# Performance work log

Hardware: AMD Instinct MI355X
Metric: run time of the kernel (lower is better)

## Reference

```python
import jax, jax.numpy as jnp
import numpy as np

NS_ITERS = 15
EPS = 1e-6


def _sqrtm(x):
    """Newton-Schulz matrix square root, 15 fixed iterations (Lin & Maji)."""
    dim = x.shape[0]
    norm = jnp.linalg.norm(x)  # Frobenius norm
    Y = x / norm
    I = jnp.eye(dim, dtype=x.dtype)
    Z = I
    for _ in range(NS_ITERS):
        T = 0.5 * (3.0 * I - Z @ Y)
        Y = Y @ T
        Z = T @ Z
    return Y * jnp.sqrt(norm)


def _gram(X):
    a, b = X.shape
    return (X @ X.T + EPS * jnp.eye(a, dtype=X.dtype)) / b


def setup_inputs() -> dict:
    key = jax.random.key(0)
    k1, k2 = jax.random.split(key)
    inp = jax.random.normal(k1, (1, 512, 256, 256), dtype=jnp.float32)
    tgt = jax.random.normal(k2, (1, 512, 256, 256), dtype=jnp.float32)
    return {"input": inp, "target_feature": tgt}


def reference(input, target_feature):
    a, b, c, d = input.shape
    n = a * b
    # --- target statistics (precomputed in __init__ of the torch module) ---
    Xt = target_feature.reshape(n, c * d)
    Mt = Xt.mean(axis=1)                     # [n]
    Gt = _gram(Xt - Mt[:, None])             # [n, n]
    sqrt_Gt = _sqrtm(Gt)                     # [n, n]
    # --- current statistics ---
    X = input.reshape(n, c * d)
    M = X.mean(axis=1)
    G = _gram(X - M[:, None])
    sqrt_G = _sqrtm(G)
    # mse(reduction='sum') on means + Bures/Wasserstein SPD distance
    loss = jnp.sum((M - Mt) ** 2)
    loss = loss + jnp.trace(G + Gt) - 2.0 * jnp.trace(sqrt_G @ sqrt_Gt)
    return loss / b
```

## Files before the change

### kernel.cpp

```cpp
#include <hip/hip_runtime.h>
#include <math.h>

#define KDIM 65536
#define MATF 262144
#define NK 16
#define CHUNK 4096
#define EPSG 1e-6

using bf16x8 = __attribute__((ext_vector_type(8))) __bf16;
using f32x4  = __attribute__((ext_vector_type(4))) float;


__global__ __launch_bounds__(256) void k_means(const float* __restrict__ X,
                                               const float* __restrict__ Xt,
                                               float* __restrict__ M) {
  const int row = blockIdx.x, inp = blockIdx.y;
  const float4* p = (const float4*)((inp ? Xt : X) + (size_t)row * KDIM);
  double s = 0.0;
  for (int i = threadIdx.x; i < KDIM / 4; i += 256) {
    float4 v = p[i];
    s += (double)v.x + (double)v.y + (double)v.z + (double)v.w;
  }
  __shared__ double sm[256];
  sm[threadIdx.x] = s;
  __syncthreads();
  for (int o = 128; o > 0; o >>= 1) {
    if (threadIdx.x < o) sm[threadIdx.x] += sm[threadIdx.x + o];
    __syncthreads();
  }
  if (threadIdx.x == 0) M[inp * 512 + row] = (float)(sm[0] * (1.0 / KDIM));
}

__device__ __forceinline__ void cvt8(float4 a, float4 b, bf16x8& hi, bf16x8& lo) {
  float f[8] = {a.x, a.y, a.z, a.w, b.x, b.y, b.z, b.w};
#pragma unroll
  for (int e = 0; e < 8; ++e) {
    __bf16 h = (__bf16)f[e];
    hi[e] = h;
    lo[e] = (__bf16)(f[e] - (float)h);
  }
}

__global__ __launch_bounds__(256, 2) void k_gram(const float* __restrict__ X,
                                                 const float* __restrict__ Xt,
                                                 float* __restrict__ Gp) {
  int rem = blockIdx.x, ti = 0;
  while (rem >= 4 - ti) { rem -= 4 - ti; ++ti; }
  const int tj = ti + rem;
  const int chunk = blockIdx.y, inp = blockIdx.z;
  const float* __restrict__ A = inp ? Xt : X;
  float* __restrict__ C = Gp + ((size_t)(inp * NK + chunk)) * MATF;
  const bool diag = (ti == tj);

  __shared__ bf16x8 AhV[512], AlV[512], BhV[512], BlV[512];

  const int t = threadIdx.x;
  const int srow = t & 127, skh = t >> 7;
  const int sbase = ((srow >> 4) << 6) + (skh << 5) + (srow & 15);

  const float* pa = A + (size_t)(ti * 128 + srow) * KDIM + (size_t)chunk * CHUNK + skh * 16;
  const float* pb = A + (size_t)(tj * 128 + srow) * KDIM + (size_t)chunk * CHUNK + skh * 16;

  const int wave = t >> 6, lane = t & 63;
  const int wy = (wave >> 1) * 64, wx = (wave & 1) * 64;

  f32x4 acc[4][4];
#pragma unroll
  for (int i = 0; i < 4; ++i)
#pragma unroll
    for (int j = 0; j < 4; ++j) acc[i][j] = (f32x4){0.f, 0.f, 0.f, 0.f};

  for (int ks = 0; ks < CHUNK; ks += 32) {
    {
      float4 v0 = *(const float4*)(pa + ks);
      float4 v1 = *(const float4*)(pa + ks + 4);
      float4 v2 = *(const float4*)(pa + ks + 8);
      float4 v3 = *(const float4*)(pa + ks + 12);
      bf16x8 h, l;
      cvt8(v0, v1, h, l); AhV[sbase] = h; AlV[sbase] = l;
      cvt8(v2, v3, h, l); AhV[sbase + 16] = h; AlV[sbase + 16] = l;
      if (!diag) {
        v0 = *(const float4*)(pb + ks);
        v1 = *(const float4*)(pb + ks + 4);
        v2 = *(const float4*)(pb + ks + 8);
        v3 = *(const float4*)(pb + ks + 12);
        cvt8(v0, v1, h, l); BhV[sbase] = h; BlV[sbase] = l;
        cvt8(v2, v3, h, l); BhV[sbase + 16] = h; BlV[sbase + 16] = l;
      }
    }
    __syncthreads();
    const bf16x8* __restrict__ Bh = diag ? AhV : BhV;
    const bf16x8* __restrict__ Bl = diag ? AlV : BlV;
    bf16x8 ah[4], al[4], bh[4], bl[4];
#pragma unroll
    for (int g = 0; g < 4; ++g) {
      ah[g] = AhV[((wave >> 1) * 4 + g) * 64 + lane];
      al[g] = AlV[((wave >> 1) * 4 + g) * 64 + lane];
      bh[g] = Bh[((wave & 1) * 4 + g) * 64 + lane];
      bl[g] = Bl[((wave & 1) * 4 + g) * 64 + lane];
    }
#pragma unroll
    for (int i = 0; i < 4; ++i)
#pragma unroll
      for (int j = 0; j < 4; ++j) {
        acc[i][j] = __builtin_amdgcn_mfma_f32_16x16x32_bf16(ah[i], bh[j], acc[i][j], 0, 0, 0);
        acc[i][j] = __builtin_amdgcn_mfma_f32_16x16x32_bf16(al[i], bh[j], acc[i][j], 0, 0, 0);
        acc[i][j] = __builtin_amdgcn_mfma_f32_16x16x32_bf16(ah[i], bl[j], acc[i][j], 0, 0, 0);
      }
    __syncthreads();
  }
  const int r4 = (lane >> 4) * 4, fc = lane & 15;
#pragma unroll
  for (int i = 0; i < 4; ++i) {
    const int grow = ti * 128 + wy + i * 16 + r4;
#pragma unroll
    for (int j = 0; j < 4; ++j) {
      const int gcol = tj * 128 + wx + j * 16 + fc;
#pragma unroll
      for (int r = 0; r < 4; ++r)
        C[(size_t)(grow + r) * 512 + gcol] = acc[i][j][r];
    }
  }
}

__global__ __launch_bounds__(256) void k_gfin(const float* __restrict__ Gp,
                                              const float* __restrict__ M,
                                              float* __restrict__ G,
                                              double* __restrict__ S) {
  const int inp = blockIdx.y;
  const int idx = blockIdx.x * 256 + threadIdx.x;
  const int i = idx >> 9, j = idx & 511;
  double n2 = 0.0, tr = 0.0;
  float* g = G + (size_t)inp * MATF;
  if (i <= j) {
    double sum = 0.0;
    const float* p = Gp + (size_t)inp * NK * MATF + idx;
#pragma unroll
    for (int c = 0; c < NK; ++c) sum += (double)p[(size_t)c * MATF];
    sum -= 65536.0 * (double)M[inp * 512 + i] * (double)M[inp * 512 + j];
    if (i == j) sum += EPSG;
    float v = (float)(sum * (1.0 / 65536.0));
    g[idx] = v;
    if (i < j) { g[(size_t)j * 512 + i] = v; n2 = 2.0 * (double)v * (double)v; }
    else       { n2 = (double)v * (double)v; tr = (double)v; }
  }
  __shared__ double s1[256], s2[256];
  s1[threadIdx.x] = n2; s2[threadIdx.x] = tr;
  __syncthreads();
  for (int o = 128; o > 0; o >>= 1) {
    if (threadIdx.x < o) { s1[threadIdx.x] += s1[threadIdx.x + o]; s2[threadIdx.x] += s2[threadIdx.x + o]; }
    __syncthreads();
  }
  if (threadIdx.x == 0) { atomicAdd(&S[inp], s1[0]); atomicAdd(&S[2 + inp], s2[0]); }
}

__global__ __launch_bounds__(256) void k_nsinit(const float* __restrict__ G,
                                                float* __restrict__ Y,
                                                float* __restrict__ Z,
                                                const double* __restrict__ S) {
  const int inp = blockIdx.y;
  const int idx = blockIdx.x * 256 + threadIdx.x;
  const float norm = (float)sqrt(S[inp]);
  Y[(size_t)(inp * 2 + 0) * MATF + idx] = G[(size_t)inp * MATF + idx] / norm;
  Y[(size_t)(inp * 2 + 1) * MATF + idx] = 0.0f;
  Z[(size_t)(inp * 2 + 0) * MATF + idx] = ((idx >> 9) == (idx & 511)) ? 1.0f : 0.0f;
  Z[(size_t)(inp * 2 + 1) * MATF + idx] = 0.0f;
}

__device__ __forceinline__ void gemm_ns(const float* __restrict__ A0, const float* __restrict__ A1,
                                        const float* __restrict__ B0, const float* __restrict__ B1,
                                        const float* __restrict__ E0, const float* __restrict__ E1,
                                        float* __restrict__ C, int k0, int mode) {
  __shared__ __align__(16) float As[64][68];
  __shared__ __align__(16) float Bs[64][68];
  const int t = threadIdx.x;
  const int tx = t & 15, ty = t >> 4;
  const int bi = blockIdx.x, bj = blockIdx.y;
  const int ar = t & 63, akq = t >> 6;
  const int bkr = t >> 2, bcs = (t & 3) * 16;

  const float* pa0 = A0 + (size_t)(bi * 64 + ar) * 512 + k0 + akq * 16;
  const float* pa1 = A1 + (size_t)(bi * 64 + ar) * 512 + k0 + akq * 16;
  const float* pb0 = B0 + (size_t)(k0 + bkr) * 512 + bj * 64 + bcs;
  const float* pb1 = B1 + (size_t)(k0 + bkr) * 512 + bj * 64 + bcs;

  float acc[4][4] = {};
  for (int ks = 0; ks < 256; ks += 64) {
#pragma unroll
    for (int q = 0; q < 4; ++q) {
      float4 va = *(const float4*)(pa0 + ks + q * 4);
      float4 vb = *(const float4*)(pa1 + ks + q * 4);
      const int kk = akq * 16 + q * 4;
      As[kk + 0][ar] = va.x + vb.x; As[kk + 1][ar] = va.y + vb.y;
      As[kk + 2][ar] = va.z + vb.z; As[kk + 3][ar] = va.w + vb.w;
    }
#pragma unroll
    for (int q = 0; q < 4; ++q) {
      float4 va = *(const float4*)(pb0 + (size_t)ks * 512 + q * 4);
      float4 vb = *(const float4*)(pb1 + (size_t)ks * 512 + q * 4);
      va.x += vb.x; va.y += vb.y; va.z += vb.z; va.w += vb.w;
      *(float4*)&Bs[bkr][bcs + q * 4] = va;
    }
    __syncthreads();
#pragma unroll 16
    for (int kk = 0; kk < 64; ++kk) {
      const float4 av = *(const float4*)&As[kk][ty << 2];
      const float4 bv = *(const float4*)&Bs[kk][tx << 2];
      acc[0][0] += av.x * bv.x; acc[0][1] += av.x * bv.y; acc[0][2] += av.x * bv.z; acc[0][3] += av.x * bv.w;
      acc[1][0] += av.y * bv.x; acc[1][1] += av.y * bv.y; acc[1][2] += av.y * bv.z; acc[1][3] += av.y * bv.w;
      acc[2][0] += av.z * bv.x; acc[2][1] += av.z * bv.y; acc[2][2] += av.z * bv.z; acc[2][3] += av.z * bv.w;
      acc[3][0] += av.w * bv.x; acc[3][1] += av.w * bv.y; acc[3][2] += av.w * bv.z; acc[3][3] += av.w * bv.w;
    }
    __syncthreads();
  }
#pragma unroll
  for (int r = 0; r < 4; ++r) {
    const int row = bi * 64 + (ty << 2) + r;
    const size_t off = (size_t)row * 512 + bj * 64 + (tx << 2);
    float4 v = make_float4(acc[r][0], acc[r][1], acc[r][2], acc[r][3]);
    if (mode != 0) {
      v.x *= -0.5f; v.y *= -0.5f; v.z *= -0.5f; v.w *= -0.5f;
      if (mode == 1) {
        float4 e0 = *(const float4*)(E0 + off);
        float4 e1 = *(const float4*)(E1 + off);
        v.x += 1.5f * (e0.x + e1.x); v.y += 1.5f * (e0.y + e1.y);
        v.z += 1.5f * (e0.z + e1.z); v.w += 1.5f * (e0.w + e1.w);
      }
    }
    *(float4*)&C[off] = v;
  }
}

__global__ __launch_bounds__(256) void k_ns_W(const float* __restrict__ Y,
                                              const float* __restrict__ Z,
                                              float* __restrict__ W) {
  const int mat = blockIdx.z >> 1, part = blockIdx.z & 1;
  const float* Zp = Z + (size_t)mat * 2 * MATF;
  const float* Yp = Y + (size_t)mat * 2 * MATF;
  gemm_ns(Zp, Zp + MATF, Yp, Yp + MATF, Yp, Yp,
          W + (size_t)(mat * 2 + part) * MATF, part * 256, 0);
}

__global__ __launch_bounds__(256) void k_ns_YZ(const float* __restrict__ Y,
                                               const float* __restrict__ Z,
                                               const float* __restrict__ W,
                                               float* __restrict__ Yn,
                                               float* __restrict__ Zn) {
  const int mat = blockIdx.z >> 2, which = (blockIdx.z >> 1) & 1, part = blockIdx.z & 1;
  const float* Yp = Y + (size_t)mat * 2 * MATF;
  const float* Zp = Z + (size_t)mat * 2 * MATF;
  const float* Wp = W + (size_t)mat * 2 * MATF;
  const int mode = (part == 0) ? 1 : 2;
  const float *a0, *a1, *b0, *b1, *e0, *e1;
  float* c;
  if (which == 0) {
    a0 = Yp; a1 = Yp + MATF; b0 = Wp; b1 = Wp + MATF; e0 = Yp; e1 = Yp + MATF;
    c = Yn + (size_t)(mat * 2 + part) * MATF;
  } else {
    a0 = Wp; a1 = Wp + MATF; b0 = Zp; b1 = Zp + MATF; e0 = Zp; e1 = Zp + MATF;
    c = Zn + (size_t)(mat * 2 + part) * MATF;
  }
  gemm_ns(a0, a1, b0, b1, e0, e1, c, part * 256, mode);
}

__global__ __launch_bounds__(256) void k_cross(const float* __restrict__ Y,
                                               double* __restrict__ S) {
  const float* YA0 = Y;            const float* YA1 = Y + MATF;
  const float* YB0 = Y + 2 * MATF; const float* YB1 = Y + 3 * MATF;
  const int base = (blockIdx.x * 256 + threadIdx.x) * 4;
  double s = 0.0;
#pragma unroll
  for (int r = 0; r < 4; ++r) {
    const int id = base + r;
    const int i = id >> 9, j = id & 511;
    const int jd = j * 512 + i;
    s += ((double)YA0[id] + (double)YA1[id]) * ((double)YB0[jd] + (double)YB1[jd]);
  }
  __shared__ double sm[256];
  sm[threadIdx.x] = s;
  __syncthreads();
  for (int o = 128; o > 0; o >>= 1) {
    if (threadIdx.x < o) sm[threadIdx.x] += sm[threadIdx.x + o];
    __syncthreads();
  }
  if (threadIdx.x == 0) atomicAdd(&S[4], sm[0]);
}

__global__ __launch_bounds__(256) void k_final(const float* __restrict__ M,
                                               const double* __restrict__ S,
                                               float* __restrict__ out) {
  double s = 0.0;
  for (int i = threadIdx.x; i < 512; i += 256) {
    double d = (double)M[i] - (double)M[512 + i];
    s += d * d;
  }
  __shared__ double sm[256];
  sm[threadIdx.x] = s;
  __syncthreads();
  for (int o = 128; o > 0; o >>= 1) {
    if (threadIdx.x < o) sm[threadIdx.x] += sm[threadIdx.x + o];
    __syncthreads();
  }
  if (threadIdx.x == 0) {
    double scale = sqrt(sqrt(S[0]) * sqrt(S[1]));
    double loss = sm[0] + S[2] + S[3] - 2.0 * scale * S[4];
    out[0] = (float)(loss / 512.0);
  }
}

extern "C" void kernel_launch(void* const* d_in, const int* in_sizes, int n_in,
                              void* d_out, int out_size, void* d_ws, size_t ws_size,
                              hipStream_t stream) {
  const float* X = (const float*)d_in[0];
  const float* Xt = (const float*)d_in[1];
  char* wsb = (char*)d_ws;
  float* Mv = (float*)wsb;
  double* S = (double*)(wsb + 4096);
  float* G = (float*)(wsb + 8192);
  float* big = (float*)(wsb + 8192 + 2 * (size_t)MATF * 4);
  float* Gp = big;
  float* Yb[2] = { big, big + 4 * (size_t)MATF };
  float* Zb[2] = { big + 8 * (size_t)MATF, big + 12 * (size_t)MATF };
  float* W = big + 16 * (size_t)MATF;

  hipMemsetAsync(S, 0, 16 * sizeof(double), stream);
  k_means<<<dim3(512, 2), 256, 0, stream>>>(X, Xt, Mv);
  k_gram<<<dim3(10, NK, 2), 256, 0, stream>>>(X, Xt, Gp);
  k_gfin<<<dim3(1024, 2), 256, 0, stream>>>(Gp, Mv, G, S);
  k_nsinit<<<dim3(1024, 2), 256, 0, stream>>>(G, Yb[0], Zb[0], S);
  int cur = 0;
  for (int it = 0; it < 15; ++it) {
    k_ns_W<<<dim3(8, 8, 4), 256, 0, stream>>>(Yb[cur], Zb[cur], W);
    k_ns_YZ<<<dim3(8, 8, 8), 256, 0, stream>>>(Yb[cur], Zb[cur], W, Yb[1 - cur], Zb[1 - cur]);
    cur ^= 1;
  }
  k_cross<<<dim3(256), 256, 0, stream>>>(Yb[cur], S);
  k_final<<<dim3(1), 256, 0, stream>>>(Mv, S, (float*)d_out);
}
```

Before: 1.416 ms.

## Fuse means into gram, prefetch loads, and run Newton-Schulz in one cooperative kernel

The separate row-mean kernel is removed: row sums are accumulated in the diagonal gram tiles and added to a global buffer with atomics. Global loads in the gram kernel are register-prefetched one step ahead. The K split doubles when the workspace is large enough. The 30 Newton-Schulz launches, together with init, cross-trace and final reduction, are replaced by one cooperative persistent kernel that uses grid.sync between phases, and the Y/Z K-split partial buffers are dropped in favour of full-K GEMMs. This removes a full read pass over the inputs and the launch overhead, at the cost of grid-wide barriers and fewer, longer-running blocks per GEMM.

```diff
diff --git a/kernel.cpp b/kernel.cpp
--- a/kernel.cpp
+++ b/kernel.cpp
@@ -1,35 +1,16 @@
 #include <hip/hip_runtime.h>
+#include <hip/hip_cooperative_groups.h>
 #include <math.h>
+
+namespace cg = cooperative_groups;
 
 #define KDIM 65536
 #define MATF 262144
-#define NK 16
-#define CHUNK 4096
 #define EPSG 1e-6
 
 using bf16x8 = __attribute__((ext_vector_type(8))) __bf16;
 using f32x4  = __attribute__((ext_vector_type(4))) float;
 
-
-__global__ __launch_bounds__(256) void k_means(const float* __restrict__ X,
-                                               const float* __restrict__ Xt,
-                                               float* __restrict__ M) {
-  const int row = blockIdx.x, inp = blockIdx.y;
-  const float4* p = (const float4*)((inp ? Xt : X) + (size_t)row * KDIM);
-  double s = 0.0;
-  for (int i = threadIdx.x; i < KDIM / 4; i += 256) {
-    float4 v = p[i];
-    s += (double)v.x + (double)v.y + (double)v.z + (double)v.w;
-  }
-  __shared__ double sm[256];
-  sm[threadIdx.x] = s;
-  __syncthreads();
-  for (int o = 128; o > 0; o >>= 1) {
-    if (threadIdx.x < o) sm[threadIdx.x] += sm[threadIdx.x + o];
-    __syncthreads();
-  }
-  if (threadIdx.x == 0) M[inp * 512 + row] = (float)(sm[0] * (1.0 / KDIM));
-}
 
 __device__ __forceinline__ void cvt8(float4 a, float4 b, bf16x8& hi, bf16x8& lo) {
   float f[8] = {a.x, a.y, a.z, a.w, b.x, b.y, b.z, b.w};
@@ -43,13 +24,15 @@
 
 __global__ __launch_bounds__(256, 2) void k_gram(const float* __restrict__ X,
                                                  const float* __restrict__ Xt,
-                                                 float* __restrict__ Gp) {
+                                                 float* __restrict__ Gp,
+                                                 double* __restrict__ Msum,
+                                                 int nk, int chunk) {
   int rem = blockIdx.x, ti = 0;
   while (rem >= 4 - ti) { rem -= 4 - ti; ++ti; }
   const int tj = ti + rem;
-  const int chunk = blockIdx.y, inp = blockIdx.z;
+  const int chunkIdx = blockIdx.y, inp = blockIdx.z;
   const float* __restrict__ A = inp ? Xt : X;
-  float* __restrict__ C = Gp + ((size_t)(inp * NK + chunk)) * MATF;
+  float* __restrict__ C = Gp + ((size_t)(inp * nk + chunkIdx)) * MATF;
   const bool diag = (ti == tj);
 
   __shared__ bf16x8 AhV[512], AlV[512], BhV[512], BlV[512];
@@ -58,8 +41,8 @@
   const int srow = t & 127, skh = t >> 7;
   const int sbase = ((srow >> 4) << 6) + (skh << 5) + (srow & 15);
 
-  const float* pa = A + (size_t)(ti * 128 + srow) * KDIM + (size_t)chunk * CHUNK + skh * 16;
-  const float* pb = A + (size_t)(tj * 128 + srow) * KDIM + (size_t)chunk * CHUNK + skh * 16;
+  const float* pa = A + (size_t)(ti * 128 + srow) * KDIM + (size_t)chunkIdx * chunk + skh * 16;
+  const float* pb = A + (size_t)(tj * 128 + srow) * KDIM + (size_t)chunkIdx * chunk + skh * 16;
 
   const int wave = t >> 6, lane = t & 63;
   const int wy = (wave >> 1) * 64, wx = (wave & 1) * 64;
@@ -70,25 +53,45 @@
 #pragma unroll
     for (int j = 0; j < 4; ++j) acc[i][j] = (f32x4){0.f, 0.f, 0.f, 0.f};
 
-  for (int ks = 0; ks < CHUNK; ks += 32) {
+  float4 ra0 = *(const float4*)(pa);
+  float4 ra1 = *(const float4*)(pa + 4);
+  float4 ra2 = *(const float4*)(pa + 8);
+  float4 ra3 = *(const float4*)(pa + 12);
+  float4 rb0, rb1, rb2, rb3;
+  if (!diag) {
+    rb0 = *(const float4*)(pb);
+    rb1 = *(const float4*)(pb + 4);
+    rb2 = *(const float4*)(pb + 8);
+    rb3 = *(const float4*)(pb + 12);
+  }
+  float rsum = 0.f;
+
+  for (int ks = 0; ks < chunk; ks += 32) {
     {
-      float4 v0 = *(const float4*)(pa + ks);
-      float4 v1 = *(const float4*)(pa + ks + 4);
-      float4 v2 = *(const float4*)(pa + ks + 8);
-      float4 v3 = *(const float4*)(pa + ks + 12);
       bf16x8 h, l;
-      cvt8(v0, v1, h, l); AhV[sbase] = h; AlV[sbase] = l;
-      cvt8(v2, v3, h, l); AhV[sbase + 16] = h; AlV[sbase + 16] = l;
+      cvt8(ra0, ra1, h, l); AhV[sbase] = h; AlV[sbase] = l;
+      cvt8(ra2, ra3, h, l); AhV[sbase + 16] = h; AlV[sbase + 16] = l;
+      if (diag) {
+        rsum += ra0.x + ra0.y + ra0.z + ra0.w + ra1.x + ra1.y + ra1.z + ra1.w +
+                ra2.x + ra2.y + ra2.z + ra2.w + ra3.x + ra3.y + ra3.z + ra3.w;
+      } else {
+        cvt8(rb0, rb1, h, l); BhV[sbase] = h; BlV[sbase] = l;
+        cvt8(rb2, rb3, h, l); BhV[sbase + 16] = h; BlV[sbase + 16] = l;
+      }
+    }
+    __syncthreads();
+    if (ks + 32 < chunk) {
+      ra0 = *(const float4*)(pa + ks + 32);
+      ra1 = *(const float4*)(pa + ks + 36);
+      ra2 = *(const float4*)(pa + ks + 40);
+      ra3 = *(const float4*)(pa + ks + 44);
       if (!diag) {
-        v0 = *(const float4*)(pb + ks);
-        v1 = *(const float4*)(pb + ks + 4);
-        v2 = *(const float4*)(pb + ks + 8);
-        v3 = *(const float4*)(pb + ks + 12);
-        cvt8(v0, v1, h, l); BhV[sbase] = h; BlV[sbase] = l;
-        cvt8(v2, v3, h, l); BhV[sbase + 16] = h; BlV[sbase + 16] = l;
-      }
-    }
-    __syncthreads();
+        rb0 = *(const float4*)(pb + ks + 32);
+        rb1 = *(const float4*)(pb + ks + 36);
+        rb2 = *(const float4*)(pb + ks + 40);
+        rb3 = *(const float4*)(pb + ks + 44);
+      }
+    }
     const bf16x8* __restrict__ Bh = diag ? AhV : BhV;
     const bf16x8* __restrict__ Bl = diag ? AlV : BlV;
     bf16x8 ah[4], al[4], bh[4], bl[4];
@@ -109,6 +112,7 @@
       }
     __syncthreads();
   }
+  if (diag) atomicAdd(&Msum[inp * 512 + ti * 128 + srow], (double)rsum);
   const int r4 = (lane >> 4) * 4, fc = lane & 15;
 #pragma unroll
   for (int i = 0; i < 4; ++i) {
@@ -124,9 +128,9 @@
 }
 
 __global__ __launch_bounds__(256) void k_gfin(const float* __restrict__ Gp,
-                                              const float* __restrict__ M,
+                                              const double* __restrict__ Msum,
                                               float* __restrict__ G,
-                                              double* __restrict__ S) {
+                                              double* __restrict__ S, int nk) {
   const int inp = blockIdx.y;
   const int idx = blockIdx.x * 256 + threadIdx.x;
   const int i = idx >> 9, j = idx & 511;
@@ -134,10 +138,9 @@
   float* g = G + (size_t)inp * MATF;
   if (i <= j) {
     double sum = 0.0;
-    const float* p = Gp + (size_t)inp * NK * MATF + idx;
-#pragma unroll
-    for (int c = 0; c < NK; ++c) sum += (double)p[(size_t)c * MATF];
-    sum -= 65536.0 * (double)M[inp * 512 + i] * (double)M[inp * 512 + j];
+    const float* p = Gp + (size_t)inp * nk * MATF + idx;
+    for (int c = 0; c < nk; ++c) sum += (double)p[(size_t)c * MATF];
+    sum -= Msum[inp * 512 + i] * Msum[inp * 512 + j] * (1.0 / 65536.0);
     if (i == j) sum += EPSG;
     float v = (float)(sum * (1.0 / 65536.0));
     g[idx] = v;
@@ -154,51 +157,41 @@
   if (threadIdx.x == 0) { atomicAdd(&S[inp], s1[0]); atomicAdd(&S[2 + inp], s2[0]); }
 }
 
-__global__ __launch_bounds__(256) void k_nsinit(const float* __restrict__ G,
-                                                float* __restrict__ Y,
-                                                float* __restrict__ Z,
-                                                const double* __restrict__ S) {
-  const int inp = blockIdx.y;
-  const int idx = blockIdx.x * 256 + threadIdx.x;
-  const float norm = (float)sqrt(S[inp]);
-  Y[(size_t)(inp * 2 + 0) * MATF + idx] = G[(size_t)inp * MATF + idx] / norm;
-  Y[(size_t)(inp * 2 + 1) * MATF + idx] = 0.0f;
-  Z[(size_t)(inp * 2 + 0) * MATF + idx] = ((idx >> 9) == (idx & 511)) ? 1.0f : 0.0f;
-  Z[(size_t)(inp * 2 + 1) * MATF + idx] = 0.0f;
-}
-
-__device__ __forceinline__ void gemm_ns(const float* __restrict__ A0, const float* __restrict__ A1,
-                                        const float* __restrict__ B0, const float* __restrict__ B1,
-                                        const float* __restrict__ E0, const float* __restrict__ E1,
-                                        float* __restrict__ C, int k0, int mode) {
-  __shared__ __align__(16) float As[64][68];
-  __shared__ __align__(16) float Bs[64][68];
+__device__ __forceinline__ void gemm64(const float* __restrict__ A0, const float* __restrict__ A1,
+                                       const float* __restrict__ B0, const float* __restrict__ B1,
+                                       const float* __restrict__ E, float* __restrict__ C,
+                                       float (*As)[68], float (*Bs)[68],
+                                       int ti, int tj, int k0, int klen, int mode) {
   const int t = threadIdx.x;
   const int tx = t & 15, ty = t >> 4;
-  const int bi = blockIdx.x, bj = blockIdx.y;
   const int ar = t & 63, akq = t >> 6;
-  const int bkr = t >> 2, bcs = (t & 3) * 16;
-
-  const float* pa0 = A0 + (size_t)(bi * 64 + ar) * 512 + k0 + akq * 16;
-  const float* pa1 = A1 + (size_t)(bi * 64 + ar) * 512 + k0 + akq * 16;
-  const float* pb0 = B0 + (size_t)(k0 + bkr) * 512 + bj * 64 + bcs;
-  const float* pb1 = B1 + (size_t)(k0 + bkr) * 512 + bj * 64 + bcs;
+  const int bkr = t >> 2, bcs = (t & 3) << 4;
+
+  const float* pa0 = A0 + (size_t)(ti * 64 + ar) * 512 + k0 + akq * 16;
+  const float* pa1 = A1 ? A1 + (size_t)(ti * 64 + ar) * 512 + k0 + akq * 16 : nullptr;
+  const float* pb0 = B0 + (size_t)(k0 + bkr) * 512 + tj * 64 + bcs;
+  const float* pb1 = B1 ? B1 + (size_t)(k0 + bkr) * 512 + tj * 64 + bcs : nullptr;
 
   float acc[4][4] = {};
-  for (int ks = 0; ks < 256; ks += 64) {
+  for (int ks = 0; ks < klen; ks += 64) {
 #pragma unroll
     for (int q = 0; q < 4; ++q) {
       float4 va = *(const float4*)(pa0 + ks + q * 4);
-      float4 vb = *(const float4*)(pa1 + ks + q * 4);
+      if (pa1) {
+        float4 vb = *(const float4*)(pa1 + ks + q * 4);
+        va.x += vb.x; va.y += vb.y; va.z += vb.z; va.w += vb.w;
+      }
       const int kk = akq * 16 + q * 4;
-      As[kk + 0][ar] = va.x + vb.x; As[kk + 1][ar] = va.y + vb.y;
-      As[kk + 2][ar] = va.z + vb.z; As[kk + 3][ar] = va.w + vb.w;
+      As[kk + 0][ar] = va.x; As[kk + 1][ar] = va.y;
+      As[kk + 2][ar] = va.z; As[kk + 3][ar] = va.w;
     }
 #pragma unroll
     for (int q = 0; q < 4; ++q) {
       float4 va = *(const float4*)(pb0 + (size_t)ks * 512 + q * 4);
-      float4 vb = *(const float4*)(pb1 + (size_t)ks * 512 + q * 4);
-      va.x += vb.x; va.y += vb.y; va.z += vb.z; va.w += vb.w;
+      if (pb1) {
+        float4 vb = *(const float4*)(pb1 + (size_t)ks * 512 + q * 4);
+        va.x += vb.x; va.y += vb.y; va.z += vb.z; va.w += vb.w;
+      }
       *(float4*)&Bs[bkr][bcs + q * 4] = va;
     }
     __syncthreads();
@@ -215,96 +208,101 @@
   }
 #pragma unroll
   for (int r = 0; r < 4; ++r) {
-    const int row = bi * 64 + (ty << 2) + r;
-    const size_t off = (size_t)row * 512 + bj * 64 + (tx << 2);
+    const int row = ti * 64 + (ty << 2) + r;
+    const size_t off = (size_t)row * 512 + tj * 64 + (tx << 2);
     float4 v = make_float4(acc[r][0], acc[r][1], acc[r][2], acc[r][3]);
-    if (mode != 0) {
-      v.x *= -0.5f; v.y *= -0.5f; v.z *= -0.5f; v.w *= -0.5f;
-      if (mode == 1) {
-        float4 e0 = *(const float4*)(E0 + off);
-        float4 e1 = *(const float4*)(E1 + off);
-        v.x += 1.5f * (e0.x + e1.x); v.y += 1.5f * (e0.y + e1.y);
-        v.z += 1.5f * (e0.z + e1.z); v.w += 1.5f * (e0.w + e1.w);
-      }
+    if (mode == 1) {
+      float4 e = *(const float4*)(E + off);
+      v.x = 1.5f * e.x - 0.5f * v.x; v.y = 1.5f * e.y - 0.5f * v.y;
+      v.z = 1.5f * e.z - 0.5f * v.z; v.w = 1.5f * e.w - 0.5f * v.w;
     }
     *(float4*)&C[off] = v;
   }
 }
 
-__global__ __launch_bounds__(256) void k_ns_W(const float* __restrict__ Y,
-                                              const float* __restrict__ Z,
-                                              float* __restrict__ W) {
-  const int mat = blockIdx.z >> 1, part = blockIdx.z & 1;
-  const float* Zp = Z + (size_t)mat * 2 * MATF;
-  const float* Yp = Y + (size_t)mat * 2 * MATF;
-  gemm_ns(Zp, Zp + MATF, Yp, Yp + MATF, Yp, Yp,
-          W + (size_t)(mat * 2 + part) * MATF, part * 256, 0);
-}
-
-__global__ __launch_bounds__(256) void k_ns_YZ(const float* __restrict__ Y,
-                                               const float* __restrict__ Z,
-                                               const float* __restrict__ W,
-                                               float* __restrict__ Yn,
-                                               float* __restrict__ Zn) {
-  const int mat = blockIdx.z >> 2, which = (blockIdx.z >> 1) & 1, part = blockIdx.z & 1;
-  const float* Yp = Y + (size_t)mat * 2 * MATF;
-  const float* Zp = Z + (size_t)mat * 2 * MATF;
-  const float* Wp = W + (size_t)mat * 2 * MATF;
-  const int mode = (part == 0) ? 1 : 2;
-  const float *a0, *a1, *b0, *b1, *e0, *e1;
-  float* c;
-  if (which == 0) {
-    a0 = Yp; a1 = Yp + MATF; b0 = Wp; b1 = Wp + MATF; e0 = Yp; e1 = Yp + MATF;
-    c = Yn + (size_t)(mat * 2 + part) * MATF;
-  } else {
-    a0 = Wp; a1 = Wp + MATF; b0 = Zp; b1 = Zp + MATF; e0 = Zp; e1 = Zp + MATF;
-    c = Zn + (size_t)(mat * 2 + part) * MATF;
-  }
-  gemm_ns(a0, a1, b0, b1, e0, e1, c, part * 256, mode);
-}
-
-__global__ __launch_bounds__(256) void k_cross(const float* __restrict__ Y,
-                                               double* __restrict__ S) {
-  const float* YA0 = Y;            const float* YA1 = Y + MATF;
-  const float* YB0 = Y + 2 * MATF; const float* YB1 = Y + 3 * MATF;
-  const int base = (blockIdx.x * 256 + threadIdx.x) * 4;
-  double s = 0.0;
-#pragma unroll
-  for (int r = 0; r < 4; ++r) {
-    const int id = base + r;
+__global__ __launch_bounds__(256) void k_ns_all(const float* __restrict__ G,
+                                                const double* __restrict__ Msum,
+                                                double* __restrict__ S,
+                                                float* __restrict__ Y0, float* __restrict__ Z0,
+                                                float* __restrict__ Y1, float* __restrict__ Z1,
+                                                float* __restrict__ W,
+                                                float* __restrict__ out) {
+  cg::grid_group grid = cg::this_grid();
+  __shared__ __align__(16) float As[64][68];
+  __shared__ __align__(16) float Bs[64][68];
+  __shared__ double sm[256];
+  const int bid = blockIdx.x, t = threadIdx.x;
+
+  {
+    const float normA = (float)sqrt(S[0]);
+    const float normB = (float)sqrt(S[1]);
+#pragma unroll
+    for (int c = 0; c < 8; ++c) {
+      const int idx = c * 65536 + bid * 256 + t;
+      const float nrm = (idx >> 18) ? normB : normA;
+      const int loc = idx & (MATF - 1);
+      Y0[idx] = G[idx] / nrm;
+      Z0[idx] = ((loc >> 9) == (loc & 511)) ? 1.0f : 0.0f;
+    }
+  }
+  grid.sync();
+
+  float *Yc = Y0, *Zc = Z0, *Yn = Y1, *Zn = Z1;
+  const int mat = bid >> 7;
+  const int sub = (bid >> 6) & 1;
+  const int tile = bid & 63, ti = tile >> 3, tj = tile & 7;
+  const size_t mo = (size_t)mat * MATF;
+
+  for (int it = 0; it < 15; ++it) {
+    gemm64(Zc + mo, nullptr, Yc + mo, nullptr, nullptr,
+           W + (size_t)(mat * 2 + sub) * MATF, As, Bs, ti, tj, sub * 256, 256, 0);
+    grid.sync();
+    const float* Wm0 = W + (size_t)mat * 2 * MATF;
+    const float* Wm1 = Wm0 + MATF;
+    if (sub == 0) {
+      gemm64(Yc + mo, nullptr, Wm0, Wm1, Yc + mo, Yn + mo, As, Bs, ti, tj, 0, 512, 1);
+    } else {
+      gemm64(Wm0, Wm1, Zc + mo, nullptr, Zc + mo, Zn + mo, As, Bs, ti, tj, 0, 512, 1);
+    }
+    grid.sync();
+    float* tp;
+    tp = Yc; Yc = Yn; Yn = tp;
+    tp = Zc; Zc = Zn; Zn = tp;
+  }
+
+  double cs = 0.0;
+#pragma unroll
+  for (int c = 0; c < 4; ++c) {
+    const int id = c * 65536 + bid * 256 + t;
     const int i = id >> 9, j = id & 511;
-    const int jd = j * 512 + i;
-    s += ((double)YA0[id] + (double)YA1[id]) * ((double)YB0[jd] + (double)YB1[jd]);
-  }
-  __shared__ double sm[256];
-  sm[threadIdx.x] = s;
+    cs += (double)Yc[id] * (double)Yc[MATF + j * 512 + i];
+  }
+  sm[t] = cs;
   __syncthreads();
   for (int o = 128; o > 0; o >>= 1) {
-    if (threadIdx.x < o) sm[threadIdx.x] += sm[threadIdx.x + o];
-    __syncthreads();
-  }
-  if (threadIdx.x == 0) atomicAdd(&S[4], sm[0]);
-}
-
-__global__ __launch_bounds__(256) void k_final(const float* __restrict__ M,
-                                               const double* __restrict__ S,
-                                               float* __restrict__ out) {
-  double s = 0.0;
-  for (int i = threadIdx.x; i < 512; i += 256) {
-    double d = (double)M[i] - (double)M[512 + i];
-    s += d * d;
-  }
-  __shared__ double sm[256];
-  sm[threadIdx.x] = s;
-  __syncthreads();
-  for (int o = 128; o > 0; o >>= 1) {
-    if (threadIdx.x < o) sm[threadIdx.x] += sm[threadIdx.x + o];
-    __syncthreads();
-  }
-  if (threadIdx.x == 0) {
-    double scale = sqrt(sqrt(S[0]) * sqrt(S[1]));
-    double loss = sm[0] + S[2] + S[3] - 2.0 * scale * S[4];
-    out[0] = (float)(loss / 512.0);
+    if (t < o) sm[t] += sm[t + o];
+    __syncthreads();
+  }
+  if (t == 0) atomicAdd(&S[4], sm[0]);
+  grid.sync();
+
+  if (bid == 0) {
+    double s = 0.0;
+    for (int i = t; i < 512; i += 256) {
+      double d = (Msum[i] - Msum[512 + i]) * (1.0 / 65536.0);
+      s += d * d;
+    }
+    sm[t] = s;
+    __syncthreads();
+    for (int o = 128; o > 0; o >>= 1) {
+      if (t < o) sm[t] += sm[t + o];
+      __syncthreads();
+    }
+    if (t == 0) {
+      double scale = sqrt(sqrt(S[0]) * sqrt(S[1]));
+      double loss = sm[0] + S[2] + S[3] - 2.0 * scale * S[4];
+      out[0] = (float)(loss / 512.0);
+    }
   }
 }
 
@@ -314,26 +312,25 @@
   const float* X = (const float*)d_in[0];
   const float* Xt = (const float*)d_in[1];
   char* wsb = (char*)d_ws;
-  float* Mv = (float*)wsb;
   double* S = (double*)(wsb + 4096);
-  float* G = (float*)(wsb + 8192);
-  float* big = (float*)(wsb + 8192 + 2 * (size_t)MATF * 4);
+  double* Msum = (double*)(wsb + 4096 + 128);
+  float* G = (float*)(wsb + 16384);
+  float* big = (float*)(wsb + 16384 + 2 * (size_t)MATF * 4);
+
+  const int nk = (ws_size >= (size_t)72 * 1024 * 1024) ? 32 : 16;
+  const int chunk = KDIM / nk;
+
   float* Gp = big;
-  float* Yb[2] = { big, big + 4 * (size_t)MATF };
-  float* Zb[2] = { big + 8 * (size_t)MATF, big + 12 * (size_t)MATF };
-  float* W = big + 16 * (size_t)MATF;
-
-  hipMemsetAsync(S, 0, 16 * sizeof(double), stream);
-  k_means<<<dim3(512, 2), 256, 0, stream>>>(X, Xt, Mv);
-  k_gram<<<dim3(10, NK, 2), 256, 0, stream>>>(X, Xt, Gp);
-  k_gfin<<<dim3(1024, 2), 256, 0, stream>>>(Gp, Mv, G, S);
-  k_nsinit<<<dim3(1024, 2), 256, 0, stream>>>(G, Yb[0], Zb[0], S);
-  int cur = 0;
-  for (int it = 0; it < 15; ++it) {
-    k_ns_W<<<dim3(8, 8, 4), 256, 0, stream>>>(Yb[cur], Zb[cur], W);
-    k_ns_YZ<<<dim3(8, 8, 8), 256, 0, stream>>>(Yb[cur], Zb[cur], W, Yb[1 - cur], Zb[1 - cur]);
-    cur ^= 1;
-  }
-  k_cross<<<dim3(256), 256, 0, stream>>>(Yb[cur], S);
-  k_final<<<dim3(1), 256, 0, stream>>>(Mv, S, (float*)d_out);
-}
+  float* Y0 = big;
+  float* Z0 = big + 2 * (size_t)MATF;
+  float* Y1 = big + 4 * (size_t)MATF;
+  float* Z1 = big + 6 * (size_t)MATF;
+  float* W  = big + 8 * (size_t)MATF;
+  float* outp = (float*)d_out;
+
+  hipMemsetAsync(S, 0, 128 + 8192, stream);
+  k_gram<<<dim3(10, nk, 2), 256, 0, stream>>>(X, Xt, Gp, Msum, nk, chunk);
+  k_gfin<<<dim3(1024, 2), 256, 0, stream>>>(Gp, Msum, G, S, nk);
+  void* args[] = {&G, &Msum, &S, &Y0, &Z0, &Y1, &Z1, &W, &outp};
+  hipLaunchCooperativeKernel((void*)k_ns_all, dim3(256), dim3(256), args, 0, stream);
+}
```

Result: slower. 2.303 ms (+62.6%).
